# Performance work log

Hardware: AMD Instinct MI355X
Metric: run time of the kernel (lower is better)

## Reference

```python
import jax, jax.numpy as jnp
import numpy as np


def _unfold(x, kh, kw):
    # torch.nn.functional.unfold ordering: channel-major, then kernel row, then kernel col
    B, C, H, W = x.shape
    Ho, Wo = H - kh + 1, W - kw + 1
    cols = jnp.stack([x[:, :, i:i + Ho, j:j + Wo]
                      for i in range(kh) for j in range(kw)], axis=2)  # [B,C,kh*kw,Ho,Wo]
    return cols.reshape(B, C * kh * kw, Ho * Wo), Ho, Wo


def _conv_unfold_matmul(x, w, b):
    # preprocessing: unfold -> A [B,L,K], B = w.view(O,-1).T [K,O]
    # matmul -> [B,L,O]; postprocessing: transpose, reshape, add bias
    O = w.shape[0]
    kh, kw = w.shape[2], w.shape[3]
    cols, Ho, Wo = _unfold(x, kh, kw)                      # [B,K,L]
    out = jnp.einsum('bkl,ok->bol', cols, w.reshape(O, -1))  # [B,O,L]
    return out.reshape(x.shape[0], O, Ho, Wo) + b[None, :, None, None]


def setup_inputs() -> dict:
    key = jax.random.key(0)
    ks = jax.random.split(key, 9)
    B = 4096
    x = jax.random.normal(ks[0], (B, 1, 28, 28), dtype=jnp.float32)
    w1 = jax.random.normal(ks[1], (10, 1, 10, 10), dtype=jnp.float32) * 0.1
    b1 = jax.random.normal(ks[2], (10,), dtype=jnp.float32) * 0.1
    w2 = jax.random.normal(ks[3], (20, 10, 10, 10), dtype=jnp.float32) * 0.03
    b2 = jax.random.normal(ks[4], (20,), dtype=jnp.float32) * 0.1
    w3 = jax.random.normal(ks[5], (20, 20, 5, 5), dtype=jnp.float32) * 0.04
    b3 = jax.random.normal(ks[6], (20,), dtype=jnp.float32) * 0.1
    wf = jax.random.normal(ks[7], (10, 720), dtype=jnp.float32) * 0.04
    bf = jax.random.normal(ks[8], (10,), dtype=jnp.float32) * 0.1
    return {"x": x, "w1": w1, "b1": b1, "w2": w2, "b2": b2,
            "w3": w3, "b3": b3, "wf": wf, "bf": bf}


def reference(x, w1, b1, w2, b2, w3, b3, wf, bf):
    h = jax.nn.relu(_conv_unfold_matmul(x, w1, b1))   # [B,10,19,19]
    h = jax.nn.relu(_conv_unfold_matmul(h, w2, b2))   # [B,20,10,10]
    h = jax.nn.relu(_conv_unfold_matmul(h, w3, b3))   # [B,20,6,6]
    h = h.reshape(-1, 720)
    return h @ wf.T + bf                               # [B,10]
```

## Files before the change

### kernel.cpp

```cpp
#include <hip/hip_runtime.h>


typedef short s16x4 __attribute__((ext_vector_type(4)));
typedef short s16x8 __attribute__((ext_vector_type(8)));
typedef float f32x4 __attribute__((ext_vector_type(4)));

#define ROW1 228
#define ROW2 248
#define H1SZ 4332
#define IMSZ 5116
#define SM_ELEMS 10232
#define XBOFF 4332

static __device__ __forceinline__ unsigned short f2bf(float f) {
    union { float f; unsigned int u; } v; v.f = f;
    unsigned int u = v.u;
    unsigned int r = (u + 0x7fffu + ((u >> 16) & 1u)) >> 16;
    return (unsigned short)r;
}

static __device__ __forceinline__ s16x8 cat8(s16x4 lo, s16x4 hi) {
    return __builtin_shufflevector(lo, hi, 0, 1, 2, 3, 4, 5, 6, 7);
}

__global__ __launch_bounds__(256) void wprep_k(const float* __restrict__ w1,
                                               const float* __restrict__ w2,
                                               const float* __restrict__ w3,
                                               unsigned short* __restrict__ wbuf) {
    int e = blockIdx.x * 256 + threadIdx.x;
    if (e < 40960) {
        int t = e & 7, lane = (e >> 3) & 63, nt = (e >> 9) & 1;
        int ck = (e >> 10) & 3, i = e >> 12;
        int k = ck * 32 + ((lane >> 4) & 3) * 8 + t;
        int o = nt * 16 + (lane & 15);
        int j = k / 12, c = k % 12;
        float val = (j < 10 && c < 10 && o < 20) ? w2[o * 1000 + c * 100 + i * 10 + j] : 0.f;
        wbuf[e] = f2bf(val);
    } else if (e < 61440) {
        int e2 = e - 40960;
        int t = e2 & 7, lane = (e2 >> 3) & 63, nt = (e2 >> 9) & 1;
        int ck = (e2 >> 10) & 3, i = e2 >> 12;
        int k = ck * 32 + ((lane >> 4) & 3) * 8 + t;
        int o = nt * 16 + (lane & 15);
        int j = k / 20, c = k % 20;
        float val = (j < 5 && o < 20) ? w3[o * 500 + c * 25 + i * 5 + j] : 0.f;
        wbuf[e] = f2bf(val);
    } else {
        int e2 = e - 61440;
        int t = e2 & 7, lane = (e2 >> 3) & 63;
        int kc = (e2 >> 9) % 9, nt = (e2 >> 9) / 9;
        int n = nt * 16 + (lane & 15);
        int k = kc * 32 + ((lane >> 4) & 3) * 8 + t;
        float val = 0.f;
        if (n < 190 && k < 280) {
            int ox = n / 10, o = n - ox * 10;
            int i = k / 28, xc = k - i * 28;
            int j = xc - ox;
            if (j >= 0 && j < 10) val = w1[o * 100 + i * 10 + j];
        }
        wbuf[61440 + e2] = f2bf(val);
    }
}

__global__ __launch_bounds__(128, 4) void fused_k(const float* __restrict__ x,
                                                  const float* __restrict__ b1,
                                                  const unsigned short* __restrict__ wbuf2,
                                                  const unsigned short* __restrict__ wbuf3,
                                                  const unsigned short* __restrict__ wband,
                                                  const float* __restrict__ b2,
                                                  const float* __restrict__ b3,
                                                  const float* __restrict__ wf,
                                                  const float* __restrict__ bf,
                                                  float* __restrict__ out) {
    __shared__ __align__(16) unsigned short sm16[SM_ELEMS];

    const int tid = threadIdx.x;
    const int wave = tid >> 6, lane = tid & 63;
    const int img = blockIdx.x * 2 + wave;
    const int quad = lane >> 4, lm = lane & 15;

    unsigned short* h1w  = sm16 + wave * IMSZ;
    unsigned short* xbfw = h1w + XBOFF;

    {
        const float4* src = (const float4*)(x + (size_t)img * 784);
        for (int k = lane; k < 196; k += 64) {
            float4 v = src[k];
            s16x4 p = { (short)f2bf(v.x), (short)f2bf(v.y),
                        (short)f2bf(v.z), (short)f2bf(v.w) };
            *(s16x4*)(xbfw + k * 4) = p;
        }
        for (int e = lane; e < 361; e += 64) {
            int oy = e / 19, ox = e - oy * 19;
            *(unsigned int*)(h1w + oy * ROW1 + ox * 12 + 10) = 0u;
        }
    }

    {
        int ab0 = lm * 28 + quad * 8;
        int r1 = lm + 16; if (r1 > 18) r1 = 18;
        int ab1 = r1 * 28 + quad * 8;
        const unsigned short* wb = wband + lane * 8;
#pragma unroll
        for (int g = 0; g < 2; ++g) {
            f32x4 acc1[6][2] = {};
#pragma unroll
            for (int kc = 0; kc < 9; ++kc) {
                s16x8 a0, a1;
                if (kc == 8 && quad == 3) {
                    a0 = (s16x8){0,0,0,0,0,0,0,0};
                    a1 = a0;
                } else {
                    a0 = cat8(*(const s16x4*)(xbfw + ab0 + kc * 32),
                              *(const s16x4*)(xbfw + ab0 + kc * 32 + 4));
                    a1 = cat8(*(const s16x4*)(xbfw + ab1 + kc * 32),
                              *(const s16x4*)(xbfw + ab1 + kc * 32 + 4));
                }
#pragma unroll
                for (int q = 0; q < 6; ++q) {
                    int nt = g * 6 + q;
                    s16x8 bw = *(const s16x8*)(wb + (nt * 9 + kc) * 512);
                    acc1[q][0] = __builtin_amdgcn_mfma_f32_16x16x32_bf16(a0, bw, acc1[q][0], 0, 0, 0);
                    acc1[q][1] = __builtin_amdgcn_mfma_f32_16x16x32_bf16(a1, bw, acc1[q][1], 0, 0, 0);
                }
            }
#pragma unroll
            for (int q = 0; q < 6; ++q) {
                int n = (g * 6 + q) * 16 + lm;
                if (n < 190) {
                    int ox = n / 10, o = n - ox * 10;
                    float bias = b1[o];
#pragma unroll
                    for (int mt = 0; mt < 2; ++mt) {
#pragma unroll
                        for (int r = 0; r < 4; ++r) {
                            int oy = mt * 16 + quad * 4 + r;
                            if (oy < 19)
                                h1w[oy * ROW1 + ox * 12 + o] =
                                    f2bf(fmaxf(acc1[q][mt][r] + bias, 0.f));
                        }
                    }
                }
            }
        }
    }

    int abase[7];
#pragma unroll
    for (int mt = 0; mt < 7; ++mt) {
        int m = mt * 16 + lm; if (m > 99) m = 99;
        int y = m / 10, xx = m - 10 * y;
        abase[mt] = y * ROW1 + xx * 12 + quad * 8;
    }
    f32x4 acc[7][2] = {};
    {
        const unsigned short* wptr = wbuf2 + lane * 8;
        s16x8 wc0 = *(const s16x8*)(wptr);
        s16x8 wc1 = *(const s16x8*)(wptr + 512);
#pragma unroll
        for (int it = 0; it < 40; ++it) {
            s16x8 wn0 = *(const s16x8*)(wptr + (it + 1) * 1024);
            s16x8 wn1 = *(const s16x8*)(wptr + (it + 1) * 1024 + 512);
            const unsigned short* sb = h1w + (it >> 2) * ROW1 + (it & 3) * 32;
            s16x8 af[7];
#pragma unroll
            for (int mt = 0; mt < 7; ++mt)
                af[mt] = cat8(*(const s16x4*)(sb + abase[mt]),
                              *(const s16x4*)(sb + abase[mt] + 4));
            __builtin_amdgcn_s_setprio(1);
#pragma unroll
            for (int mt = 0; mt < 7; ++mt) {
                acc[mt][0] = __builtin_amdgcn_mfma_f32_16x16x32_bf16(af[mt], wc0, acc[mt][0], 0, 0, 0);
                acc[mt][1] = __builtin_amdgcn_mfma_f32_16x16x32_bf16(af[mt], wc1, acc[mt][1], 0, 0, 0);
            }
            __builtin_amdgcn_s_setprio(0);
            wc0 = wn0; wc1 = wn1;
        }
    }

    unsigned short* h2w = h1w;
#pragma unroll
    for (int mt = 0; mt < 7; ++mt) {
#pragma unroll
        for (int nt = 0; nt < 2; ++nt) {
            int o = nt * 16 + lm;
            if (o < 20) {
                float bias = b2[o];
#pragma unroll
                for (int r = 0; r < 4; ++r) {
                    int pos = mt * 16 + quad * 4 + r;
                    if (pos < 100) {
                        int y2 = pos / 10, x2 = pos - 10 * y2;
                        h2w[y2 * ROW2 + x2 * 20 + o] =
                            f2bf(fmaxf(acc[mt][nt][r] + bias, 0.f));
                    }
                }
            }
        }
    }

    int abase3[3];
#pragma unroll
    for (int mt = 0; mt < 3; ++mt) {
        int m = mt * 16 + lm; if (m > 35) m = 35;
        int oy = m / 6, ox = m - 6 * oy;
        abase3[mt] = oy * ROW2 + ox * 20 + quad * 8;
    }
    f32x4 acc3[3][2] = {};
    {
        const unsigned short* wptr = wbuf3 + lane * 8;
        s16x8 wc0 = *(const s16x8*)(wptr);
        s16x8 wc1 = *(const s16x8*)(wptr + 512);
#pragma unroll
        for (int it = 0; it < 20; ++it) {
            s16x8 wn0 = *(const s16x8*)(wptr + (it + 1) * 1024);
            s16x8 wn1 = *(const s16x8*)(wptr + (it + 1) * 1024 + 512);
            const unsigned short* sb = h2w + (it >> 2) * ROW2 + (it & 3) * 32;
            s16x8 af[3];
#pragma unroll
            for (int mt = 0; mt < 3; ++mt)
                af[mt] = cat8(*(const s16x4*)(sb + abase3[mt]),
                              *(const s16x4*)(sb + abase3[mt] + 4));
            __builtin_amdgcn_s_setprio(1);
#pragma unroll
            for (int mt = 0; mt < 3; ++mt) {
                acc3[mt][0] = __builtin_amdgcn_mfma_f32_16x16x32_bf16(af[mt], wc0, acc3[mt][0], 0, 0, 0);
                acc3[mt][1] = __builtin_amdgcn_mfma_f32_16x16x32_bf16(af[mt], wc1, acc3[mt][1], 0, 0, 0);
            }
            __builtin_amdgcn_s_setprio(0);
            wc0 = wn0; wc1 = wn1;
        }
    }

    float* h3w = (float*)h1w;
#pragma unroll
    for (int mt = 0; mt < 3; ++mt) {
#pragma unroll
        for (int nt = 0; nt < 2; ++nt) {
            int o = nt * 16 + lm;
            if (o < 20) {
                float b3v = b3[o];
#pragma unroll
                for (int r = 0; r < 4; ++r) {
                    int pos = mt * 16 + quad * 4 + r;
                    if (pos < 36)
                        h3w[o * 36 + pos] = fmaxf(acc3[mt][nt][r] + b3v, 0.f);
                }
            }
        }
    }

    float part[10];
#pragma unroll
    for (int n = 0; n < 10; ++n) part[n] = 0.f;
#pragma unroll 2
    for (int s = 0; s < 11; ++s) {
        int k = s * 64 + lane;
        float v = h3w[k];
#pragma unroll
        for (int n = 0; n < 10; ++n)
            part[n] = fmaf(v, wf[n * 720 + k], part[n]);
    }
    {
        int k = 704 + lane;
        if (lane < 16) {
            float v = h3w[k];
#pragma unroll
            for (int n = 0; n < 10; ++n)
                part[n] = fmaf(v, wf[n * 720 + k], part[n]);
        }
    }
#pragma unroll
    for (int n = 0; n < 10; ++n) {
#pragma unroll
        for (int off = 32; off >= 1; off >>= 1)
            part[n] += __shfl_xor(part[n], off, 64);
    }
    if (lane == 0) {
        float* dst = out + (size_t)img * 10;
#pragma unroll
        for (int n = 0; n < 10; ++n) dst[n] = part[n] + bf[n];
    }
}

extern "C" void kernel_launch(void* const* d_in, const int* in_sizes, int n_in,
                              void* d_out, int out_size, void* d_ws, size_t ws_size,
                              hipStream_t stream) {
    (void)n_in; (void)out_size; (void)ws_size;
    const float* x  = (const float*)d_in[0];
    const float* w1 = (const float*)d_in[1];
    const float* b1 = (const float*)d_in[2];
    const float* w2 = (const float*)d_in[3];
    const float* b2 = (const float*)d_in[4];
    const float* w3 = (const float*)d_in[5];
    const float* b3 = (const float*)d_in[6];
    const float* wf = (const float*)d_in[7];
    const float* bf = (const float*)d_in[8];
    float* out = (float*)d_out;

    const int B = in_sizes[0] / 784;

    unsigned short* wbuf = (unsigned short*)d_ws;

    wprep_k<<<456, 256, 0, stream>>>(w1, w2, w3, wbuf);
    fused_k<<<B / 2, 128, 0, stream>>>(x, b1, wbuf, wbuf + 40960, wbuf + 61440,
                                       b2, b3, wf, bf, out);
}
```

Measured before the change: 145.7 us.

## Process two images per wave with deeper register prefetch of weights and activations

Each wave now handles two images (img and img+B/2), loading both inputs up front and looping, which halves the grid size. Weight fragments are prefetched three iterations ahead in a 4-deep register ring, and the next iteration's LDS A-fragments are double-buffered in all conv stages. The ROW1 pitch is widened to 248 with explicit zeroing of the tail padding. Launch bounds drop to 2 blocks/SM so the larger register footprint fits, which trades occupancy for per-wave latency hiding.

```diff
diff --git a/kernel.cpp b/kernel.cpp
--- a/kernel.cpp
+++ b/kernel.cpp
@@ -5,12 +5,12 @@
 typedef short s16x8 __attribute__((ext_vector_type(8)));
 typedef float f32x4 __attribute__((ext_vector_type(4)));
 
-#define ROW1 228
+#define ROW1 248
 #define ROW2 248
-#define H1SZ 4332
-#define IMSZ 5116
-#define SM_ELEMS 10232
-#define XBOFF 4332
+#define H1SZ 4712
+#define XBSZ 800
+#define IMSZ 6312
+#define SM_ELEMS 12624
 
 static __device__ __forceinline__ unsigned short f2bf(float f) {
     union { float f; unsigned int u; } v; v.f = f;
@@ -62,7 +62,7 @@
     }
 }
 
-__global__ __launch_bounds__(128, 4) void fused_k(const float* __restrict__ x,
+__global__ __launch_bounds__(128, 2) void fused_k(const float* __restrict__ x,
                                                   const float* __restrict__ b1,
                                                   const unsigned short* __restrict__ wbuf2,
                                                   const unsigned short* __restrict__ wbuf3,
@@ -71,215 +71,262 @@
                                                   const float* __restrict__ b3,
                                                   const float* __restrict__ wf,
                                                   const float* __restrict__ bf,
-                                                  float* __restrict__ out) {
+                                                  float* __restrict__ out,
+                                                  int half) {
     __shared__ __align__(16) unsigned short sm16[SM_ELEMS];
 
     const int tid = threadIdx.x;
     const int wave = tid >> 6, lane = tid & 63;
-    const int img = blockIdx.x * 2 + wave;
     const int quad = lane >> 4, lm = lane & 15;
-
-    unsigned short* h1w  = sm16 + wave * IMSZ;
-    unsigned short* xbfw = h1w + XBOFF;
-
-    {
-        const float4* src = (const float4*)(x + (size_t)img * 784);
+    const int img0 = blockIdx.x * 2 + wave;
+
+    unsigned short* h1w = sm16 + wave * IMSZ;
+    unsigned short* xb2 = h1w + H1SZ;
+
+#pragma unroll
+    for (int s2 = 0; s2 < 2; ++s2) {
+        const float4* src = (const float4*)(x + (size_t)(img0 + s2 * half) * 784);
+        unsigned short* dst = xb2 + s2 * XBSZ;
         for (int k = lane; k < 196; k += 64) {
             float4 v = src[k];
             s16x4 p = { (short)f2bf(v.x), (short)f2bf(v.y),
                         (short)f2bf(v.z), (short)f2bf(v.w) };
-            *(s16x4*)(xbfw + k * 4) = p;
+            *(s16x4*)(dst + k * 4) = p;
+        }
+    }
+    if (lane < 32) xb2[(lane >> 4) * XBSZ + 784 + (lane & 15)] = 0;
+
+#pragma unroll 1
+    for (int s = 0; s < 2; ++s) {
+        const unsigned short* xbfw = xb2 + s * XBSZ;
+        const int img = img0 + s * half;
+
+        for (int e = lane; e < 95; e += 64) {
+            int row = e / 5, seg = e - row * 5;
+            *(s16x4*)(h1w + row * ROW1 + 228 + seg * 4) = (s16x4){0, 0, 0, 0};
         }
         for (int e = lane; e < 361; e += 64) {
             int oy = e / 19, ox = e - oy * 19;
             *(unsigned int*)(h1w + oy * ROW1 + ox * 12 + 10) = 0u;
         }
-    }
-
-    {
-        int ab0 = lm * 28 + quad * 8;
-        int r1 = lm + 16; if (r1 > 18) r1 = 18;
-        int ab1 = r1 * 28 + quad * 8;
-        const unsigned short* wb = wband + lane * 8;
-#pragma unroll
-        for (int g = 0; g < 2; ++g) {
-            f32x4 acc1[6][2] = {};
-#pragma unroll
-            for (int kc = 0; kc < 9; ++kc) {
-                s16x8 a0, a1;
-                if (kc == 8 && quad == 3) {
-                    a0 = (s16x8){0,0,0,0,0,0,0,0};
-                    a1 = a0;
-                } else {
-                    a0 = cat8(*(const s16x4*)(xbfw + ab0 + kc * 32),
-                              *(const s16x4*)(xbfw + ab0 + kc * 32 + 4));
-                    a1 = cat8(*(const s16x4*)(xbfw + ab1 + kc * 32),
-                              *(const s16x4*)(xbfw + ab1 + kc * 32 + 4));
+
+        {
+            int ab0 = lm * 28 + quad * 8;
+            int r1 = lm + 16; if (r1 > 18) r1 = 18;
+            int ab1 = r1 * 28 + quad * 8;
+            const unsigned short* wb = wband + lane * 8;
+#pragma unroll
+            for (int g = 0; g < 2; ++g) {
+                f32x4 acc1[6][2] = {};
+                s16x8 wr[4][6];
+#pragma unroll
+                for (int d = 0; d < 3; ++d)
+#pragma unroll
+                    for (int q = 0; q < 6; ++q)
+                        wr[d][q] = *(const s16x8*)(wb + (((g * 6 + q) * 9) + d) * 512);
+#pragma unroll
+                for (int kc = 0; kc < 9; ++kc) {
+                    if (kc < 6) {
+#pragma unroll
+                        for (int q = 0; q < 6; ++q)
+                            wr[(kc + 3) & 3][q] =
+                                *(const s16x8*)(wb + (((g * 6 + q) * 9) + kc + 3) * 512);
+                    }
+                    s16x8 a0 = cat8(*(const s16x4*)(xbfw + ab0 + kc * 32),
+                                    *(const s16x4*)(xbfw + ab0 + kc * 32 + 4));
+                    s16x8 a1 = cat8(*(const s16x4*)(xbfw + ab1 + kc * 32),
+                                    *(const s16x4*)(xbfw + ab1 + kc * 32 + 4));
+                    __builtin_amdgcn_s_setprio(1);
+#pragma unroll
+                    for (int q = 0; q < 6; ++q) {
+                        acc1[q][0] = __builtin_amdgcn_mfma_f32_16x16x32_bf16(a0, wr[kc & 3][q], acc1[q][0], 0, 0, 0);
+                        acc1[q][1] = __builtin_amdgcn_mfma_f32_16x16x32_bf16(a1, wr[kc & 3][q], acc1[q][1], 0, 0, 0);
+                    }
+                    __builtin_amdgcn_s_setprio(0);
                 }
 #pragma unroll
                 for (int q = 0; q < 6; ++q) {
-                    int nt = g * 6 + q;
-                    s16x8 bw = *(const s16x8*)(wb + (nt * 9 + kc) * 512);
-                    acc1[q][0] = __builtin_amdgcn_mfma_f32_16x16x32_bf16(a0, bw, acc1[q][0], 0, 0, 0);
-                    acc1[q][1] = __builtin_amdgcn_mfma_f32_16x16x32_bf16(a1, bw, acc1[q][1], 0, 0, 0);
-                }
-            }
-#pragma unroll
-            for (int q = 0; q < 6; ++q) {
-                int n = (g * 6 + q) * 16 + lm;
-                if (n < 190) {
-                    int ox = n / 10, o = n - ox * 10;
-                    float bias = b1[o];
-#pragma unroll
-                    for (int mt = 0; mt < 2; ++mt) {
-#pragma unroll
-                        for (int r = 0; r < 4; ++r) {
-                            int oy = mt * 16 + quad * 4 + r;
-                            if (oy < 19)
-                                h1w[oy * ROW1 + ox * 12 + o] =
-                                    f2bf(fmaxf(acc1[q][mt][r] + bias, 0.f));
+                    int n = (g * 6 + q) * 16 + lm;
+                    if (n < 190) {
+                        int ox = n / 10, o = n - ox * 10;
+                        float bias = b1[o];
+#pragma unroll
+                        for (int mt = 0; mt < 2; ++mt) {
+#pragma unroll
+                            for (int r = 0; r < 4; ++r) {
+                                int oy = mt * 16 + quad * 4 + r;
+                                if (oy < 19)
+                                    h1w[oy * ROW1 + ox * 12 + o] =
+                                        f2bf(fmaxf(acc1[q][mt][r] + bias, 0.f));
+                            }
                         }
                     }
                 }
             }
         }
-    }
-
-    int abase[7];
-#pragma unroll
-    for (int mt = 0; mt < 7; ++mt) {
-        int m = mt * 16 + lm; if (m > 99) m = 99;
-        int y = m / 10, xx = m - 10 * y;
-        abase[mt] = y * ROW1 + xx * 12 + quad * 8;
-    }
-    f32x4 acc[7][2] = {};
-    {
-        const unsigned short* wptr = wbuf2 + lane * 8;
-        s16x8 wc0 = *(const s16x8*)(wptr);
-        s16x8 wc1 = *(const s16x8*)(wptr + 512);
-#pragma unroll
-        for (int it = 0; it < 40; ++it) {
-            s16x8 wn0 = *(const s16x8*)(wptr + (it + 1) * 1024);
-            s16x8 wn1 = *(const s16x8*)(wptr + (it + 1) * 1024 + 512);
-            const unsigned short* sb = h1w + (it >> 2) * ROW1 + (it & 3) * 32;
-            s16x8 af[7];
+
+        int abase[7];
+#pragma unroll
+        for (int mt = 0; mt < 7; ++mt) {
+            int m = mt * 16 + lm; if (m > 99) m = 99;
+            int y = m / 10, xx = m - 10 * y;
+            abase[mt] = y * ROW1 + xx * 12 + quad * 8;
+        }
+        f32x4 acc[7][2] = {};
+        {
+            const unsigned short* wptr = wbuf2 + lane * 8;
+            s16x8 w0r[4], w1r[4];
+#pragma unroll
+            for (int d = 0; d < 3; ++d) {
+                w0r[d] = *(const s16x8*)(wptr + d * 1024);
+                w1r[d] = *(const s16x8*)(wptr + d * 1024 + 512);
+            }
+            s16x8 afc[7], afn[7];
 #pragma unroll
             for (int mt = 0; mt < 7; ++mt)
-                af[mt] = cat8(*(const s16x4*)(sb + abase[mt]),
-                              *(const s16x4*)(sb + abase[mt] + 4));
-            __builtin_amdgcn_s_setprio(1);
-#pragma unroll
-            for (int mt = 0; mt < 7; ++mt) {
-                acc[mt][0] = __builtin_amdgcn_mfma_f32_16x16x32_bf16(af[mt], wc0, acc[mt][0], 0, 0, 0);
-                acc[mt][1] = __builtin_amdgcn_mfma_f32_16x16x32_bf16(af[mt], wc1, acc[mt][1], 0, 0, 0);
-            }
-            __builtin_amdgcn_s_setprio(0);
-            wc0 = wn0; wc1 = wn1;
-        }
-    }
-
-    unsigned short* h2w = h1w;
-#pragma unroll
-    for (int mt = 0; mt < 7; ++mt) {
-#pragma unroll
-        for (int nt = 0; nt < 2; ++nt) {
-            int o = nt * 16 + lm;
-            if (o < 20) {
-                float bias = b2[o];
-#pragma unroll
-                for (int r = 0; r < 4; ++r) {
-                    int pos = mt * 16 + quad * 4 + r;
-                    if (pos < 100) {
-                        int y2 = pos / 10, x2 = pos - 10 * y2;
-                        h2w[y2 * ROW2 + x2 * 20 + o] =
-                            f2bf(fmaxf(acc[mt][nt][r] + bias, 0.f));
-                    }
-                }
-            }
-        }
-    }
-
-    int abase3[3];
-#pragma unroll
-    for (int mt = 0; mt < 3; ++mt) {
-        int m = mt * 16 + lm; if (m > 35) m = 35;
-        int oy = m / 6, ox = m - 6 * oy;
-        abase3[mt] = oy * ROW2 + ox * 20 + quad * 8;
-    }
-    f32x4 acc3[3][2] = {};
-    {
-        const unsigned short* wptr = wbuf3 + lane * 8;
-        s16x8 wc0 = *(const s16x8*)(wptr);
-        s16x8 wc1 = *(const s16x8*)(wptr + 512);
-#pragma unroll
-        for (int it = 0; it < 20; ++it) {
-            s16x8 wn0 = *(const s16x8*)(wptr + (it + 1) * 1024);
-            s16x8 wn1 = *(const s16x8*)(wptr + (it + 1) * 1024 + 512);
-            const unsigned short* sb = h2w + (it >> 2) * ROW2 + (it & 3) * 32;
-            s16x8 af[3];
+                afc[mt] = cat8(*(const s16x4*)(h1w + abase[mt]),
+                               *(const s16x4*)(h1w + abase[mt] + 4));
+#pragma unroll
+            for (int it = 0; it < 40; ++it) {
+                if (it < 37) {
+                    w0r[(it + 3) & 3] = *(const s16x8*)(wptr + (it + 3) * 1024);
+                    w1r[(it + 3) & 3] = *(const s16x8*)(wptr + (it + 3) * 1024 + 512);
+                }
+                if (it < 39) {
+                    const unsigned short* sbn = h1w + ((it + 1) >> 2) * ROW1 + ((it + 1) & 3) * 32;
+#pragma unroll
+                    for (int mt = 0; mt < 7; ++mt)
+                        afn[mt] = cat8(*(const s16x4*)(sbn + abase[mt]),
+                                       *(const s16x4*)(sbn + abase[mt] + 4));
+                }
+                __builtin_amdgcn_s_setprio(1);
+#pragma unroll
+                for (int mt = 0; mt < 7; ++mt) {
+                    acc[mt][0] = __builtin_amdgcn_mfma_f32_16x16x32_bf16(afc[mt], w0r[it & 3], acc[mt][0], 0, 0, 0);
+                    acc[mt][1] = __builtin_amdgcn_mfma_f32_16x16x32_bf16(afc[mt], w1r[it & 3], acc[mt][1], 0, 0, 0);
+                }
+                __builtin_amdgcn_s_setprio(0);
+#pragma unroll
+                for (int mt = 0; mt < 7; ++mt) afc[mt] = afn[mt];
+            }
+        }
+
+        unsigned short* h2w = h1w;
+#pragma unroll
+        for (int mt = 0; mt < 7; ++mt) {
+#pragma unroll
+            for (int nt = 0; nt < 2; ++nt) {
+                int o = nt * 16 + lm;
+                if (o < 20) {
+                    float bias = b2[o];
+#pragma unroll
+                    for (int r = 0; r < 4; ++r) {
+                        int pos = mt * 16 + quad * 4 + r;
+                        if (pos < 100) {
+                            int y2 = pos / 10, x2 = pos - 10 * y2;
+                            h2w[y2 * ROW2 + x2 * 20 + o] =
+                                f2bf(fmaxf(acc[mt][nt][r] + bias, 0.f));
+                        }
+                    }
+                }
+            }
+        }
+
+        int abase3[3];
+#pragma unroll
+        for (int mt = 0; mt < 3; ++mt) {
+            int m = mt * 16 + lm; if (m > 35) m = 35;
+            int oy = m / 6, ox = m - 6 * oy;
+            abase3[mt] = oy * ROW2 + ox * 20 + quad * 8;
+        }
+        f32x4 acc3[3][2] = {};
+        {
+            const unsigned short* wptr = wbuf3 + lane * 8;
+            s16x8 w0r[4], w1r[4];
+#pragma unroll
+            for (int d = 0; d < 3; ++d) {
+                w0r[d] = *(const s16x8*)(wptr + d * 1024);
+                w1r[d] = *(const s16x8*)(wptr + d * 1024 + 512);
+            }
+            s16x8 afc[3], afn[3];
 #pragma unroll
             for (int mt = 0; mt < 3; ++mt)
-                af[mt] = cat8(*(const s16x4*)(sb + abase3[mt]),
-                              *(const s16x4*)(sb + abase3[mt] + 4));
-            __builtin_amdgcn_s_setprio(1);
-#pragma unroll
-            for (int mt = 0; mt < 3; ++mt) {
-                acc3[mt][0] = __builtin_amdgcn_mfma_f32_16x16x32_bf16(af[mt], wc0, acc3[mt][0], 0, 0, 0);
-                acc3[mt][1] = __builtin_amdgcn_mfma_f32_16x16x32_bf16(af[mt], wc1, acc3[mt][1], 0, 0, 0);
-            }
-            __builtin_amdgcn_s_setprio(0);
-            wc0 = wn0; wc1 = wn1;
-        }
-    }
-
-    float* h3w = (float*)h1w;
-#pragma unroll
-    for (int mt = 0; mt < 3; ++mt) {
-#pragma unroll
-        for (int nt = 0; nt < 2; ++nt) {
-            int o = nt * 16 + lm;
-            if (o < 20) {
-                float b3v = b3[o];
-#pragma unroll
-                for (int r = 0; r < 4; ++r) {
-                    int pos = mt * 16 + quad * 4 + r;
-                    if (pos < 36)
-                        h3w[o * 36 + pos] = fmaxf(acc3[mt][nt][r] + b3v, 0.f);
-                }
-            }
-        }
-    }
-
-    float part[10];
-#pragma unroll
-    for (int n = 0; n < 10; ++n) part[n] = 0.f;
+                afc[mt] = cat8(*(const s16x4*)(h2w + abase3[mt]),
+                               *(const s16x4*)(h2w + abase3[mt] + 4));
+#pragma unroll
+            for (int it = 0; it < 20; ++it) {
+                if (it < 17) {
+                    w0r[(it + 3) & 3] = *(const s16x8*)(wptr + (it + 3) * 1024);
+                    w1r[(it + 3) & 3] = *(const s16x8*)(wptr + (it + 3) * 1024 + 512);
+                }
+                if (it < 19) {
+                    const unsigned short* sbn = h2w + ((it + 1) >> 2) * ROW2 + ((it + 1) & 3) * 32;
+#pragma unroll
+                    for (int mt = 0; mt < 3; ++mt)
+                        afn[mt] = cat8(*(const s16x4*)(sbn + abase3[mt]),
+                                       *(const s16x4*)(sbn + abase3[mt] + 4));
+                }
+                __builtin_amdgcn_s_setprio(1);
+#pragma unroll
+                for (int mt = 0; mt < 3; ++mt) {
+                    acc3[mt][0] = __builtin_amdgcn_mfma_f32_16x16x32_bf16(afc[mt], w0r[it & 3], acc3[mt][0], 0, 0, 0);
+                    acc3[mt][1] = __builtin_amdgcn_mfma_f32_16x16x32_bf16(afc[mt], w1r[it & 3], acc3[mt][1], 0, 0, 0);
+                }
+                __builtin_amdgcn_s_setprio(0);
+#pragma unroll
+                for (int mt = 0; mt < 3; ++mt) afc[mt] = afn[mt];
+            }
+        }
+
+        float* h3w = (float*)h1w;
+#pragma unroll
+        for (int mt = 0; mt < 3; ++mt) {
+#pragma unroll
+            for (int nt = 0; nt < 2; ++nt) {
+                int o = nt * 16 + lm;
+                if (o < 20) {
+                    float b3v = b3[o];
+#pragma unroll
+                    for (int r = 0; r < 4; ++r) {
+                        int pos = mt * 16 + quad * 4 + r;
+                        if (pos < 36)
+                            h3w[o * 36 + pos] = fmaxf(acc3[mt][nt][r] + b3v, 0.f);
+                    }
+                }
+            }
+        }
+
+        float part[10];
+#pragma unroll
+        for (int n = 0; n < 10; ++n) part[n] = 0.f;
 #pragma unroll 2
-    for (int s = 0; s < 11; ++s) {
-        int k = s * 64 + lane;
-        float v = h3w[k];
-#pragma unroll
-        for (int n = 0; n < 10; ++n)
-            part[n] = fmaf(v, wf[n * 720 + k], part[n]);
-    }
-    {
-        int k = 704 + lane;
-        if (lane < 16) {
+        for (int t = 0; t < 11; ++t) {
+            int k = t * 64 + lane;
             float v = h3w[k];
 #pragma unroll
             for (int n = 0; n < 10; ++n)
                 part[n] = fmaf(v, wf[n * 720 + k], part[n]);
         }
-    }
-#pragma unroll
-    for (int n = 0; n < 10; ++n) {
-#pragma unroll
-        for (int off = 32; off >= 1; off >>= 1)
-            part[n] += __shfl_xor(part[n], off, 64);
-    }
-    if (lane == 0) {
-        float* dst = out + (size_t)img * 10;
-#pragma unroll
-        for (int n = 0; n < 10; ++n) dst[n] = part[n] + bf[n];
+        {
+            int k = 704 + lane;
+            if (lane < 16) {
+                float v = h3w[k];
+#pragma unroll
+                for (int n = 0; n < 10; ++n)
+                    part[n] = fmaf(v, wf[n * 720 + k], part[n]);
+            }
+        }
+#pragma unroll
+        for (int n = 0; n < 10; ++n) {
+#pragma unroll
+            for (int off = 32; off >= 1; off >>= 1)
+                part[n] += __shfl_xor(part[n], off, 64);
+        }
+        if (lane == 0) {
+            float* dst = out + (size_t)img * 10;
+#pragma unroll
+            for (int n = 0; n < 10; ++n) dst[n] = part[n] + bf[n];
+        }
     }
 }
 
@@ -299,10 +346,11 @@
     float* out = (float*)d_out;
 
     const int B = in_sizes[0] / 784;
+    const int half = B / 2;
 
     unsigned short* wbuf = (unsigned short*)d_ws;
 
     wprep_k<<<456, 256, 0, stream>>>(w1, w2, w3, wbuf);
-    fused_k<<<B / 2, 128, 0, stream>>>(x, b1, wbuf, wbuf + 40960, wbuf + 61440,
-                                       b2, b3, wf, bf, out);
-}
+    fused_k<<<B / 4, 128, 0, stream>>>(x, b1, wbuf, wbuf + 40960, wbuf + 61440,
+                                       b2, b3, wf, bf, out, half);
+}
```

Result: slower. 542.3 us (+272.2%).

## Stream conv1 input from global with prefetch, drop LDS staging of image

Applied to the files above, without the earlier changes.

Conv1 A-operands are now read straight from global fp32 input and converted to bf16 in registers, with the next k-chunk prefetched. This removes the LDS copy of the image and shrinks shared memory per block, which may allow more blocks per CU. Weight fragments are software-pipelined one step ahead, and MFMA issue is wrapped in s_setprio. The h1 row stride is widened, with the padding zeroed. Risks include redundant global loads (L1/L2-bound), more register pressure, and the quad-3 zeroing for kc=8 being replaced by clamped reads, which relies on zero padding in the weights.

```diff
diff --git a/kernel.cpp b/kernel.cpp
--- a/kernel.cpp
+++ b/kernel.cpp
@@ -5,12 +5,10 @@
 typedef short s16x8 __attribute__((ext_vector_type(8)));
 typedef float f32x4 __attribute__((ext_vector_type(4)));
 
-#define ROW1 228
+#define ROW1 248
 #define ROW2 248
-#define H1SZ 4332
-#define IMSZ 5116
-#define SM_ELEMS 10232
-#define XBOFF 4332
+#define H1SZ 4712
+#define SM_ELEMS 9424
 
 static __device__ __forceinline__ unsigned short f2bf(float f) {
     union { float f; unsigned int u; } v; v.f = f;
@@ -21,6 +19,15 @@
 
 static __device__ __forceinline__ s16x8 cat8(s16x4 lo, s16x4 hi) {
     return __builtin_shufflevector(lo, hi, 0, 1, 2, 3, 4, 5, 6, 7);
+}
+
+static __device__ __forceinline__ s16x8 f2bf8(f32x4 a, f32x4 b) {
+    s16x8 r;
+    r[0] = (short)f2bf(a[0]); r[1] = (short)f2bf(a[1]);
+    r[2] = (short)f2bf(a[2]); r[3] = (short)f2bf(a[3]);
+    r[4] = (short)f2bf(b[0]); r[5] = (short)f2bf(b[1]);
+    r[6] = (short)f2bf(b[2]); r[7] = (short)f2bf(b[3]);
+    return r;
 }
 
 __global__ __launch_bounds__(256) void wprep_k(const float* __restrict__ w1,
@@ -76,53 +83,60 @@
 
     const int tid = threadIdx.x;
     const int wave = tid >> 6, lane = tid & 63;
+    const int quad = lane >> 4, lm = lane & 15;
     const int img = blockIdx.x * 2 + wave;
-    const int quad = lane >> 4, lm = lane & 15;
-
-    unsigned short* h1w  = sm16 + wave * IMSZ;
-    unsigned short* xbfw = h1w + XBOFF;
+
+    unsigned short* h1w = sm16 + wave * H1SZ;
+
+    for (int e = lane; e < 95; e += 64) {
+        int row = e / 5, seg = e - row * 5;
+        *(s16x4*)(h1w + row * ROW1 + 228 + seg * 4) = (s16x4){0, 0, 0, 0};
+    }
+    for (int e = lane; e < 361; e += 64) {
+        int oy = e / 19, ox = e - oy * 19;
+        *(unsigned int*)(h1w + oy * ROW1 + ox * 12 + 10) = 0u;
+    }
 
     {
-        const float4* src = (const float4*)(x + (size_t)img * 784);
-        for (int k = lane; k < 196; k += 64) {
-            float4 v = src[k];
-            s16x4 p = { (short)f2bf(v.x), (short)f2bf(v.y),
-                        (short)f2bf(v.z), (short)f2bf(v.w) };
-            *(s16x4*)(xbfw + k * 4) = p;
-        }
-        for (int e = lane; e < 361; e += 64) {
-            int oy = e / 19, ox = e - oy * 19;
-            *(unsigned int*)(h1w + oy * ROW1 + ox * 12 + 10) = 0u;
-        }
-    }
-
-    {
-        int ab0 = lm * 28 + quad * 8;
+        const float* xg = x + (size_t)img * 784;
+        const int ab0 = lm * 28 + quad * 8;
         int r1 = lm + 16; if (r1 > 18) r1 = 18;
-        int ab1 = r1 * 28 + quad * 8;
+        const int ab1 = r1 * 28 + quad * 8;
         const unsigned short* wb = wband + lane * 8;
-#pragma unroll
+#pragma unroll 1
         for (int g = 0; g < 2; ++g) {
             f32x4 acc1[6][2] = {};
+            f32x4 c0a = *(const f32x4*)(xg + ab0);
+            f32x4 c0b = *(const f32x4*)(xg + ab0 + 4);
+            f32x4 c1a = *(const f32x4*)(xg + ab1);
+            f32x4 c1b = *(const f32x4*)(xg + ab1 + 4);
 #pragma unroll
             for (int kc = 0; kc < 9; ++kc) {
-                s16x8 a0, a1;
-                if (kc == 8 && quad == 3) {
-                    a0 = (s16x8){0,0,0,0,0,0,0,0};
-                    a1 = a0;
-                } else {
-                    a0 = cat8(*(const s16x4*)(xbfw + ab0 + kc * 32),
-                              *(const s16x4*)(xbfw + ab0 + kc * 32 + 4));
-                    a1 = cat8(*(const s16x4*)(xbfw + ab1 + kc * 32),
-                              *(const s16x4*)(xbfw + ab1 + kc * 32 + 4));
-                }
+                f32x4 n0a, n0b, n1a, n1b;
+                if (kc < 8) {
+                    int of0 = ab0 + (kc + 1) * 32;
+                    int of1 = ab1 + (kc + 1) * 32;
+                    if (of1 > 776) of1 = 776;
+                    n0a = *(const f32x4*)(xg + of0);
+                    n0b = *(const f32x4*)(xg + of0 + 4);
+                    n1a = *(const f32x4*)(xg + of1);
+                    n1b = *(const f32x4*)(xg + of1 + 4);
+                }
+                s16x8 a0 = f2bf8(c0a, c0b);
+                s16x8 a1 = f2bf8(c1a, c1b);
+                s16x8 wq = *(const s16x8*)(wb + (((g * 6) * 9) + kc) * 512);
+                __builtin_amdgcn_s_setprio(1);
 #pragma unroll
                 for (int q = 0; q < 6; ++q) {
-                    int nt = g * 6 + q;
-                    s16x8 bw = *(const s16x8*)(wb + (nt * 9 + kc) * 512);
-                    acc1[q][0] = __builtin_amdgcn_mfma_f32_16x16x32_bf16(a0, bw, acc1[q][0], 0, 0, 0);
-                    acc1[q][1] = __builtin_amdgcn_mfma_f32_16x16x32_bf16(a1, bw, acc1[q][1], 0, 0, 0);
-                }
+                    s16x8 wn;
+                    if (q < 5)
+                        wn = *(const s16x8*)(wb + (((g * 6 + q + 1) * 9) + kc) * 512);
+                    acc1[q][0] = __builtin_amdgcn_mfma_f32_16x16x32_bf16(a0, wq, acc1[q][0], 0, 0, 0);
+                    acc1[q][1] = __builtin_amdgcn_mfma_f32_16x16x32_bf16(a1, wq, acc1[q][1], 0, 0, 0);
+                    if (q < 5) wq = wn;
+                }
+                __builtin_amdgcn_s_setprio(0);
+                c0a = n0a; c0b = n0b; c1a = n1a; c1b = n1b;
             }
 #pragma unroll
             for (int q = 0; q < 6; ++q) {
@@ -254,8 +268,8 @@
 #pragma unroll
     for (int n = 0; n < 10; ++n) part[n] = 0.f;
 #pragma unroll 2
-    for (int s = 0; s < 11; ++s) {
-        int k = s * 64 + lane;
+    for (int t = 0; t < 11; ++t) {
+        int k = t * 64 + lane;
         float v = h3w[k];
 #pragma unroll
         for (int n = 0; n < 10; ++n)
```

Measured after the change: 156.6 us. +7.5%, slower.
